# Performance work log

Hardware: AMD Instinct MI355X
Metric: run time of the kernel (lower is better)

Reference implementation:

```python
import jax, jax.numpy as jnp
import numpy as np

EMB_DIM = 1024
NUM_HEADS = 16
HEAD_DIM = EMB_DIM // NUM_HEADS


def setup_inputs() -> dict:
    key = jax.random.key(0)
    ks = jax.random.split(key, 9)
    B, S = 2, 2048
    s = 1.0 / np.sqrt(EMB_DIM)
    return {
        "x": jax.random.normal(ks[0], (B, S, EMB_DIM), jnp.float32),
        "Wq": jax.random.normal(ks[1], (EMB_DIM, EMB_DIM), jnp.float32) * s,
        "bq": jnp.zeros((EMB_DIM,), jnp.float32),
        "Wk": jax.random.normal(ks[2], (EMB_DIM, EMB_DIM), jnp.float32) * s,
        "bk": jnp.zeros((EMB_DIM,), jnp.float32),
        "Wv": jax.random.normal(ks[3], (EMB_DIM, EMB_DIM), jnp.float32) * s,
        "bv": jnp.zeros((EMB_DIM,), jnp.float32),
        "Wo": jax.random.normal(ks[4], (EMB_DIM, EMB_DIM), jnp.float32) * s,
        "bo": jnp.zeros((EMB_DIM,), jnp.float32),
    }


def reference(x, Wq, bq, Wk, bk, Wv, bv, Wo, bo):
    B, S, E = x.shape
    H, D = NUM_HEADS, HEAD_DIM
    # QKV projections (torch Linear: x @ W.T + b; here W is stored as [in,out])
    q = (x @ Wq + bq).reshape(B, S, H, D).transpose(0, 2, 1, 3)  # [B,H,S,D]
    k = (x @ Wk + bk).reshape(B, S, H, D).transpose(0, 2, 1, 3)
    v = (x @ Wv + bv).reshape(B, S, H, D).transpose(0, 2, 1, 3)
    # raw scores, then causal mask with -inf, then scale inside softmax
    scores = jnp.einsum("bhqd,bhkd->bhqk", q, k)  # [B,H,S,S]
    causal = jnp.tril(jnp.ones((S, S), bool))
    scores = jnp.where(causal, scores, -jnp.inf)
    attn = jax.nn.softmax(scores / np.sqrt(D), axis=-1)
    # dropout prob is 0.0 (eval-equivalent), so it's identity
    ctx = jnp.einsum("bhqk,bhkd->bhqd", attn, v)  # [B,H,S,D]
    ctx = ctx.transpose(0, 2, 1, 3).reshape(B, S, E)
    return ctx @ Wo + bo
```

## Files before the change

### kernel.cpp

```cpp
#include <hip/hip_runtime.h>
#include <hip/hip_bf16.h>
#include <cstdint>

#define NB   2
#define NS   2048
#define NE   1024
#define NH   16
#define ND   64
#define BS   (NB*NS)

typedef float f32x4 __attribute__((ext_vector_type(4)));
typedef __bf16 bf16x8 __attribute__((ext_vector_type(8)));

#define MFMA16(a,b,c) __builtin_amdgcn_mfma_f32_16x16x32_bf16((a),(b),(c),0,0,0)

#define KCF 0.18033688011112042f

typedef const __attribute__((address_space(1))) unsigned int* gas_u32;
typedef __attribute__((address_space(3))) unsigned int* las_u32;

__device__ __forceinline__ void gload_lds16(const void* g, void* l) {
    __builtin_amdgcn_global_load_lds((gas_u32)g, (las_u32)l, 16, 0, 0);
}

__device__ __forceinline__ unsigned short bf16_bits(float f) {
    __bf16 h = (__bf16)f;
    return __builtin_bit_cast(unsigned short, h);
}
__device__ __forceinline__ float bits_bf16(unsigned short u) {
    return (float)__builtin_bit_cast(__bf16, u);
}

__global__ __launch_bounds__(256) void prep_kernel(const float* __restrict__ x,
                                                   __bf16* __restrict__ xb,
                                                   const float* __restrict__ W0,
                                                   const float* __restrict__ W1,
                                                   const float* __restrict__ W2,
                                                   const float* __restrict__ W3,
                                                   __bf16* __restrict__ wt) {
    __shared__ float tile[32][33];
    int z = blockIdx.z;
    int tx = threadIdx.x, ty = threadIdx.y;
    if (z == 0) {
        size_t base = ((size_t)(blockIdx.y * 32 + blockIdx.x) * 256 +
                       ty * 32 + tx) * 16;
        const float4* p = (const float4*)(x + base);
        float4 a = p[0], b = p[1], c = p[2], d = p[3];
        bf16x8 v0, v1;
        v0[0]=(__bf16)a.x; v0[1]=(__bf16)a.y; v0[2]=(__bf16)a.z; v0[3]=(__bf16)a.w;
        v0[4]=(__bf16)b.x; v0[5]=(__bf16)b.y; v0[6]=(__bf16)b.z; v0[7]=(__bf16)b.w;
        v1[0]=(__bf16)c.x; v1[1]=(__bf16)c.y; v1[2]=(__bf16)c.z; v1[3]=(__bf16)c.w;
        v1[4]=(__bf16)d.x; v1[5]=(__bf16)d.y; v1[6]=(__bf16)d.z; v1[7]=(__bf16)d.w;
        *(bf16x8*)(xb + base) = v0;
        *(bf16x8*)(xb + base + 8) = v1;
        return;
    }
    int w = z - 1;
    const float* W = (w==0) ? W0 : (w==1) ? W1 : (w==2) ? W2 : W3;
    __bf16* out = wt + (size_t)w * NE * NE;
    int k0 = blockIdx.y * 32, n0 = blockIdx.x * 32;
    #pragma unroll
    for (int i = 0; i < 4; i++)
        tile[ty + 8*i][tx] = W[(size_t)(k0 + ty + 8*i) * NE + n0 + tx];
    __syncthreads();
    #pragma unroll
    for (int i = 0; i < 4; i++)
        out[(size_t)(n0 + ty + 8*i) * NE + k0 + tx] = (__bf16)tile[tx][ty + 8*i];
}

template<int EPI>
__global__ __launch_bounds__(256, 2) void gemm128_kernel(
        const __bf16* __restrict__ A, const __bf16* __restrict__ Bt,
        const float* __restrict__ bias0, const float* __restrict__ bias1,
        const float* __restrict__ bias2,
        __bf16* __restrict__ o0, __bf16* __restrict__ o1, __bf16* __restrict__ o2,
        float* __restrict__ fout) {
    __shared__ __align__(16) char smem[2][16384];
    const int K = 1024;
    int t = threadIdx.x;
    int wave = t >> 6, lane = t & 63;
    int wm = wave >> 1, wn = wave & 1;
    int lg = lane >> 4, li = lane & 15;

    int bid = blockIdx.y * gridDim.x + blockIdx.x;
    int cpx = (gridDim.x * gridDim.y) >> 3;
    int swzb = (bid & 7) * cpx + (bid >> 3);
    int m0 = (swzb / gridDim.x) * 128, n0 = (swzb % gridDim.x) * 128;

    const __bf16* Ag = A + (size_t)(m0 + (t >> 2)) * K + (t & 3) * 8;
    const __bf16* Bg = Bt + (size_t)(n0 + (t >> 2)) * K + (t & 3) * 8;

#define GSTAGE(K0, BI) do {                                             \
        gload_lds16(Ag + (K0),          smem[BI] +         t * 16);     \
        gload_lds16(Ag + 64 * K + (K0), smem[BI] +  4096 + t * 16);     \
        gload_lds16(Bg + (K0),          smem[BI] +  8192 + t * 16);     \
        gload_lds16(Bg + 64 * K + (K0), smem[BI] + 12288 + t * 16);     \
    } while (0)

    GSTAGE(0, 0);
    f32x4 acc[4][4] = {};
    __syncthreads();

    for (int k0 = 0; k0 < K; k0 += 32) {
        int cur = (k0 >> 5) & 1;
        if (k0 + 32 < K) {
            GSTAGE(k0 + 32, cur ^ 1);
            asm volatile("s_waitcnt vmcnt(4)" ::: "memory");
        } else {
            asm volatile("s_waitcnt vmcnt(0)" ::: "memory");
        }
        __builtin_amdgcn_s_barrier();

        const __bf16* As = (const __bf16*)smem[cur];
        const __bf16* Bs = (const __bf16*)(smem[cur] + 8192);
        bf16x8 af[4], bfr[4];
        #pragma unroll
        for (int i = 0; i < 4; i++)
            af[i] = *(const bf16x8*)(As + (size_t)(wm*64 + i*16 + li) * 32 + lg * 8);
        #pragma unroll
        for (int i = 0; i < 4; i++)
            bfr[i] = *(const bf16x8*)(Bs + (size_t)(wn*64 + i*16 + li) * 32 + lg * 8);
        #pragma unroll
        for (int i = 0; i < 4; i++)
            #pragma unroll
            for (int j = 0; j < 4; j++)
                acc[i][j] = MFMA16(af[i], bfr[j], acc[i][j]);

        asm volatile("s_waitcnt lgkmcnt(0)" ::: "memory");
        __builtin_amdgcn_sched_barrier(0);
        __builtin_amdgcn_s_barrier();
    }
#undef GSTAGE

    #pragma unroll
    for (int i = 0; i < 4; i++) {
        int mrow = m0 + wm * 64 + i * 16 + lg * 4;
        #pragma unroll
        for (int j = 0; j < 4; j++) {
            int n = n0 + wn * 64 + j * 16 + li;
            if (EPI == 0) {
                int widx = n >> 10, nn = n & 1023;
                const float* bb = (widx == 0) ? bias0 : (widx == 1) ? bias1 : bias2;
                float bv = bb[nn];
                int h = nn >> 6, d = nn & 63;
                int bidx = mrow >> 11, s0 = mrow & 2047;
                if (widx == 2) {
                    ushort4 pk;
                    pk.x = bf16_bits(acc[i][j][0] + bv);
                    pk.y = bf16_bits(acc[i][j][1] + bv);
                    pk.z = bf16_bits(acc[i][j][2] + bv);
                    pk.w = bf16_bits(acc[i][j][3] + bv);
                    *(ushort4*)(o2 + (((size_t)bidx * NH + h) * ND + d) * NS + s0) = pk;
                } else {
                    __bf16* dst = (widx == 0) ? o0 : o1;
                    float scl = (widx == 0) ? KCF : 1.0f;
                    #pragma unroll
                    for (int r = 0; r < 4; r++)
                        dst[(((size_t)bidx * NH + h) * NS + s0 + r) * ND + d] =
                            (__bf16)((acc[i][j][r] + bv) * scl);
                }
            } else {
                float bv = bias0[n];
                #pragma unroll
                for (int r = 0; r < 4; r++)
                    fout[(size_t)(mrow + r) * NE + n] = acc[i][j][r] + bv;
            }
        }
    }
}

__global__ __launch_bounds__(256) void attn_kernel(const __bf16* __restrict__ qb,
                                                   const __bf16* __restrict__ kb,
                                                   const __bf16* __restrict__ vt,
                                                   __bf16* __restrict__ ctx,
                                                   __bf16* __restrict__ Opart,
                                                   float* __restrict__ lbuf,
                                                   int split) {
    __shared__ __align__(16) char kbuf[2][8192];
    __shared__ __align__(16) char vbuf[2][8192];
    __shared__ __align__(16) ushort pbuf[4][1024];

    int t = threadIdx.x;
    int wave = t >> 6, lane = t & 63;
    int lg = lane >> 4, li = lane & 15;
    int bh = blockIdx.y, b = bh >> 4, h = bh & 15;
    int bx = (split ? 79 : 31) - blockIdx.x;

    int qt, c, nch;
    if (!split) {
        qt = bx; c = 0; nch = 1;
    } else {
        int a = (bx < 8) ? 0 : (bx < 24) ? 1 : (bx < 48) ? 2 : 3;
        int seg = (a == 0) ? 0 : (a == 1) ? 8 : (a == 2) ? 24 : 48;
        int idx = bx - seg;
        int dv = a + 1;
        qt = a * 8 + idx / dv;
        c  = idx % dv;
        nch = a + 1;
    }
    int jlo = c * 8;
    int jhi = min(jlo + 8, qt + 1);
    int nt = jhi - jlo;
    bool direct = (nch == 1);

    int qw = qt * 64 + wave * 16;
    const __bf16* Q  = qb + ((size_t)bh * NS + qw) * ND;
    const __bf16* Kg = kb + (size_t)bh * NS * ND;
    const __bf16* Vg = vt + (size_t)bh * ND * NS;

    int sr = t >> 3;
    int sg = (t & 7) ^ (sr & 7);
    const __bf16* Ks0 = Kg + (size_t)sr * ND + sg * 8;
    const __bf16* Ks1 = Kg + (size_t)(32 + sr) * ND + sg * 8;
    const __bf16* Vs0 = Vg + (size_t)sr * NS + sg * 8;
    const __bf16* Vs1 = Vg + (size_t)(32 + sr) * NS + sg * 8;

#define STAGE_KV(J, BI) do {                                              \
        gload_lds16(Ks0 + (size_t)(J) * 4096, &kbuf[BI][t * 16]);         \
        gload_lds16(Ks1 + (size_t)(J) * 4096, &kbuf[BI][4096 + t * 16]);  \
        gload_lds16(Vs0 + (size_t)(J) * 64,   &vbuf[BI][t * 16]);         \
        gload_lds16(Vs1 + (size_t)(J) * 64,   &vbuf[BI][4096 + t * 16]);  \
    } while (0)

    bf16x8 aq0 = *(const bf16x8*)(Q + li * ND + lg * 8);
    bf16x8 aq1 = *(const bf16x8*)(Q + li * ND + 32 + lg * 8);

    STAGE_KV(jlo, 0);

    f32x4 o[4] = {};
    float lpart = 0.f;
    int swz = (li & 7) << 4;
    int qg = qw + li;

    char* pw = (char*)&pbuf[wave][0];
    char* pwr = pw + li * 128 + (lg & 1) * 8;
    int k6base = (lg >> 1);

    __syncthreads();

    for (int it = 0; it < nt; ++it) {
        int j = jlo + it;
        int cur = it & 1;
        if (it + 1 < nt) {
            STAGE_KV(j + 1, cur ^ 1);
            asm volatile("s_waitcnt vmcnt(4)" ::: "memory");
        } else {
            asm volatile("s_waitcnt vmcnt(0)" ::: "memory");
        }
        __builtin_amdgcn_s_barrier();

        const char* kt = (const char*)kbuf[cur];
        f32x4 sc[4];
        __builtin_amdgcn_s_setprio(1);
        #pragma unroll
        for (int h4 = 0; h4 < 4; ++h4) {
            const char* kr = kt + (h4 * 16 + li) * 128;
            bf16x8 b0 = *(const bf16x8*)(kr + ((lg << 4) ^ swz));
            bf16x8 b1 = *(const bf16x8*)(kr + (((4 + lg) << 4) ^ swz));
            f32x4 z = {};
            z = MFMA16(b0, aq0, z);
            z = MFMA16(b1, aq1, z);
            sc[h4] = z;
        }
        __builtin_amdgcn_s_setprio(0);

        if (j == qt) {
            #pragma unroll
            for (int h4 = 0; h4 < 4; ++h4)
                #pragma unroll
                for (int r = 0; r < 4; ++r) {
                    int kv = j * 64 + h4 * 16 + lg * 4 + r;
                    if (kv > qg) sc[h4][r] = -1e30f;
                }
        }

        #pragma unroll
        for (int h4 = 0; h4 < 4; ++h4) {
            #pragma unroll
            for (int r = 0; r < 4; ++r) {
                float p = exp2f(sc[h4][r]);
                sc[h4][r] = p;
                lpart += p;
            }
        }

        #pragma unroll
        for (int h4 = 0; h4 < 4; ++h4) {
            uint2 w64;
            w64.x = (unsigned int)bf16_bits(sc[h4][0]) |
                    ((unsigned int)bf16_bits(sc[h4][1]) << 16);
            w64.y = (unsigned int)bf16_bits(sc[h4][2]) |
                    ((unsigned int)bf16_bits(sc[h4][3]) << 16);
            int k6 = h4 * 2 + k6base;
            *(uint2*)(pwr + (((k6 ^ (li & 7)) << 4))) = w64;
        }
        asm volatile("s_waitcnt lgkmcnt(0)" ::: "memory");
        __builtin_amdgcn_sched_barrier(0);

        const char* vtl = (const char*)vbuf[cur];
        __builtin_amdgcn_s_setprio(1);
        #pragma unroll
        for (int ks = 0; ks < 2; ++ks) {
            int ch = (ks * 4 + lg) << 4;
            bf16x8 pf = *(const bf16x8*)(pw + li * 128 + (ch ^ swz));
            #pragma unroll
            for (int i = 0; i < 4; ++i) {
                bf16x8 vf = *(const bf16x8*)(vtl + (i * 16 + li) * 128 + (ch ^ swz));
                o[i] = MFMA16(vf, pf, o[i]);
            }
        }
        __builtin_amdgcn_s_setprio(0);

        asm volatile("s_waitcnt lgkmcnt(0)" ::: "memory");
        __builtin_amdgcn_sched_barrier(0);
        __builtin_amdgcn_s_barrier();
    }
#undef STAGE_KV

    float lsum = lpart + __shfl_xor(lpart, 16);
    lsum += __shfl_xor(lsum, 32);

    if (direct) {
        float inv = 1.f / lsum;
        __bf16* dst = ctx + ((size_t)b * NS + qg) * NE + h * ND;
        #pragma unroll
        for (int i = 0; i < 4; ++i) {
            ushort4 pack;
            pack.x = bf16_bits(o[i][0] * inv);
            pack.y = bf16_bits(o[i][1] * inv);
            pack.z = bf16_bits(o[i][2] * inv);
            pack.w = bf16_bits(o[i][3] * inv);
            *(ushort4*)(dst + i * 16 + lg * 4) = pack;
        }
    } else {
        int slot = bh * 80 + bx;
        int ql = wave * 16 + li;
        __bf16* Op = Opart + (size_t)slot * 4096 + ql * 64;
        #pragma unroll
        for (int i = 0; i < 4; ++i) {
            ushort4 pack;
            pack.x = bf16_bits(o[i][0]);
            pack.y = bf16_bits(o[i][1]);
            pack.z = bf16_bits(o[i][2]);
            pack.w = bf16_bits(o[i][3]);
            *(ushort4*)(Op + i * 16 + lg * 4) = pack;
        }
        if (lg == 0)
            lbuf[(size_t)slot * 64 + ql] = lsum;
    }
}

__global__ __launch_bounds__(256) void combine_kernel(const __bf16* __restrict__ Opart,
                                                      const float* __restrict__ lbuf,
                                                      __bf16* __restrict__ ctx) {
    int qt = 8 + blockIdx.x;
    int bh = blockIdx.y, b = bh >> 4, h = bh & 15;
    int a = qt >> 3, bq = qt & 7;
    int off = (a + 1) * (4 * a + bq);
    int nch = a + 1;
    int slotbase = bh * 80 + off;
    int t = threadIdx.x;
    int q = t >> 2, dg = t & 3;

    float L = 0.f;
    #pragma unroll
    for (int c = 0; c < 4; ++c)
        if (c < nch)
            L += lbuf[(size_t)(slotbase + c) * 64 + q];
    float invL = 1.f / L;

    float acc[16] = {};
    #pragma unroll
    for (int c = 0; c < 4; ++c)
        if (c < nch) {
            const uint4* src = (const uint4*)(Opart + (size_t)(slotbase + c) * 4096 +
                                              q * 64 + dg * 16);
            #pragma unroll
            for (int half = 0; half < 2; ++half) {
                uint4 v = src[half];
                unsigned int w[4] = {v.x, v.y, v.z, v.w};
                #pragma unroll
                for (int u = 0; u < 4; ++u) {
                    acc[half * 8 + u * 2]     += bits_bf16((ushort)(w[u] & 0xffff));
                    acc[half * 8 + u * 2 + 1] += bits_bf16((ushort)(w[u] >> 16));
                }
            }
        }

    int qg = qt * 64 + q;
    __bf16* dst = ctx + ((size_t)b * NS + qg) * NE + h * ND + dg * 16;
    #pragma unroll
    for (int half = 0; half < 2; ++half) {
        ushort4 pack;
        pack.x = bf16_bits(acc[half * 8 + 0] * invL);
        pack.y = bf16_bits(acc[half * 8 + 1] * invL);
        pack.z = bf16_bits(acc[half * 8 + 2] * invL);
        pack.w = bf16_bits(acc[half * 8 + 3] * invL);
        ushort4 pack2;
        pack2.x = bf16_bits(acc[half * 8 + 4] * invL);
        pack2.y = bf16_bits(acc[half * 8 + 5] * invL);
        pack2.z = bf16_bits(acc[half * 8 + 6] * invL);
        pack2.w = bf16_bits(acc[half * 8 + 7] * invL);
        *(ushort4*)(dst + half * 8) = pack;
        *(ushort4*)(dst + half * 8 + 4) = pack2;
    }
}

extern "C" void kernel_launch(void* const* d_in, const int* in_sizes, int n_in,
                              void* d_out, int out_size, void* d_ws, size_t ws_size,
                              hipStream_t stream) {
    (void)in_sizes; (void)n_in; (void)out_size;
    const float* x  = (const float*)d_in[0];
    const float* Wq = (const float*)d_in[1];
    const float* bq = (const float*)d_in[2];
    const float* Wk = (const float*)d_in[3];
    const float* bk = (const float*)d_in[4];
    const float* Wv = (const float*)d_in[5];
    const float* bv = (const float*)d_in[6];
    const float* Wo = (const float*)d_in[7];
    const float* bo = (const float*)d_in[8];
    float* out = (float*)d_out;

    char* ws = (char*)d_ws;
    const size_t MB = 1024 * 1024;
    __bf16* xb  = (__bf16*)(ws);
    __bf16* wt  = (__bf16*)(ws +  8 * MB);
    __bf16* qb  = (__bf16*)(ws + 16 * MB);
    __bf16* kb  = (__bf16*)(ws + 24 * MB);
    __bf16* vtb = (__bf16*)(ws + 32 * MB);
    __bf16* ctx = xb;
    __bf16* Opart = (__bf16*)(ws + 40 * MB);
    float*  lbuf  = (float*)(ws + 40 * MB + 20971520);
    const size_t NEED = 40 * MB + 20971520 + 655360;

    int split = (ws_size >= NEED) ? 1 : 0;

    prep_kernel<<<dim3(32, 32, 5), dim3(32, 8), 0, stream>>>(
        x, xb, Wq, Wk, Wv, Wo, wt);
    gemm128_kernel<0><<<dim3(24, 32), 256, 0, stream>>>(
        xb, wt, bq, bk, bv, qb, kb, vtb, nullptr);
    attn_kernel<<<dim3(split ? 80 : 32, NB * NH), 256, 0, stream>>>(
        qb, kb, vtb, ctx, Opart, lbuf, split);
    if (split)
        combine_kernel<<<dim3(24, NB * NH), 256, 0, stream>>>(Opart, lbuf, ctx);
    gemm128_kernel<1><<<dim3(8, 32), 256, 0, stream>>>(
        ctx, wt + 3 * (size_t)NE * NE, bo, nullptr, nullptr, nullptr, nullptr,
        nullptr, out);
}
```

Measured before the change: 194.8 us.

## Double attention query tile per wave and split out-projection into 64-row GEMM

The attention kernel now processes 128 query rows per block (32 per wave, two MFMA row groups), so each staged K/V tile is reused across twice as many queries. The split-KV scheme, partial buffers and combine kernel are resized to match, and the causal mask test now checks each tile against the wave's rows. The output projection gets its own 64x128-tile GEMM kernel, which launches twice as many blocks to fill more CUs. The trade-off is higher register and LDS use in attention, fewer attention blocks, and more masked work on the diagonal tiles.

```diff
diff --git a/kernel.cpp b/kernel.cpp
--- a/kernel.cpp
+++ b/kernel.cpp
@@ -68,13 +68,11 @@
         out[(size_t)(n0 + ty + 8*i) * NE + k0 + tx] = (__bf16)tile[tx][ty + 8*i];
 }
 
-template<int EPI>
-__global__ __launch_bounds__(256, 2) void gemm128_kernel(
+__global__ __launch_bounds__(256, 2) void gemm_qkv_kernel(
         const __bf16* __restrict__ A, const __bf16* __restrict__ Bt,
         const float* __restrict__ bias0, const float* __restrict__ bias1,
         const float* __restrict__ bias2,
-        __bf16* __restrict__ o0, __bf16* __restrict__ o1, __bf16* __restrict__ o2,
-        float* __restrict__ fout) {
+        __bf16* __restrict__ o0, __bf16* __restrict__ o1, __bf16* __restrict__ o2) {
     __shared__ __align__(16) char smem[2][16384];
     const int K = 1024;
     int t = threadIdx.x;
@@ -138,33 +136,98 @@
         #pragma unroll
         for (int j = 0; j < 4; j++) {
             int n = n0 + wn * 64 + j * 16 + li;
-            if (EPI == 0) {
-                int widx = n >> 10, nn = n & 1023;
-                const float* bb = (widx == 0) ? bias0 : (widx == 1) ? bias1 : bias2;
-                float bv = bb[nn];
-                int h = nn >> 6, d = nn & 63;
-                int bidx = mrow >> 11, s0 = mrow & 2047;
-                if (widx == 2) {
-                    ushort4 pk;
-                    pk.x = bf16_bits(acc[i][j][0] + bv);
-                    pk.y = bf16_bits(acc[i][j][1] + bv);
-                    pk.z = bf16_bits(acc[i][j][2] + bv);
-                    pk.w = bf16_bits(acc[i][j][3] + bv);
-                    *(ushort4*)(o2 + (((size_t)bidx * NH + h) * ND + d) * NS + s0) = pk;
-                } else {
-                    __bf16* dst = (widx == 0) ? o0 : o1;
-                    float scl = (widx == 0) ? KCF : 1.0f;
-                    #pragma unroll
-                    for (int r = 0; r < 4; r++)
-                        dst[(((size_t)bidx * NH + h) * NS + s0 + r) * ND + d] =
-                            (__bf16)((acc[i][j][r] + bv) * scl);
-                }
+            int widx = n >> 10, nn = n & 1023;
+            const float* bb = (widx == 0) ? bias0 : (widx == 1) ? bias1 : bias2;
+            float bv = bb[nn];
+            int h = nn >> 6, d = nn & 63;
+            int bidx = mrow >> 11, s0 = mrow & 2047;
+            if (widx == 2) {
+                ushort4 pk;
+                pk.x = bf16_bits(acc[i][j][0] + bv);
+                pk.y = bf16_bits(acc[i][j][1] + bv);
+                pk.z = bf16_bits(acc[i][j][2] + bv);
+                pk.w = bf16_bits(acc[i][j][3] + bv);
+                *(ushort4*)(o2 + (((size_t)bidx * NH + h) * ND + d) * NS + s0) = pk;
             } else {
-                float bv = bias0[n];
+                __bf16* dst = (widx == 0) ? o0 : o1;
+                float scl = (widx == 0) ? KCF : 1.0f;
                 #pragma unroll
                 for (int r = 0; r < 4; r++)
-                    fout[(size_t)(mrow + r) * NE + n] = acc[i][j][r] + bv;
-            }
+                    dst[(((size_t)bidx * NH + h) * NS + s0 + r) * ND + d] =
+                        (__bf16)((acc[i][j][r] + bv) * scl);
+            }
+        }
+    }
+}
+
+__global__ __launch_bounds__(256, 2) void gemm_out_kernel(
+        const __bf16* __restrict__ A, const __bf16* __restrict__ Bt,
+        const float* __restrict__ bias, float* __restrict__ fout) {
+    __shared__ __align__(16) char smem[2][12288];
+    const int K = 1024;
+    int t = threadIdx.x;
+    int wave = t >> 6, lane = t & 63;
+    int lg = lane >> 4, li = lane & 15;
+
+    int bid = blockIdx.y * gridDim.x + blockIdx.x;
+    int cpx = (gridDim.x * gridDim.y) >> 3;
+    int swzb = (bid & 7) * cpx + (bid >> 3);
+    int m0 = (swzb / gridDim.x) * 64, n0 = (swzb % gridDim.x) * 128;
+
+    const __bf16* Ag = A + (size_t)(m0 + (t >> 2)) * K + (t & 3) * 8;
+    const __bf16* Bg = Bt + (size_t)(n0 + (t >> 2)) * K + (t & 3) * 8;
+
+#define GSTAGE(K0, BI) do {                                             \
+        gload_lds16(Ag + (K0),          smem[BI] +         t * 16);     \
+        gload_lds16(Bg + (K0),          smem[BI] +  4096 + t * 16);     \
+        gload_lds16(Bg + 64 * K + (K0), smem[BI] +  8192 + t * 16);     \
+    } while (0)
+
+    GSTAGE(0, 0);
+    f32x4 acc[4][2] = {};
+    __syncthreads();
+
+    for (int k0 = 0; k0 < K; k0 += 32) {
+        int cur = (k0 >> 5) & 1;
+        if (k0 + 32 < K) {
+            GSTAGE(k0 + 32, cur ^ 1);
+            asm volatile("s_waitcnt vmcnt(3)" ::: "memory");
+        } else {
+            asm volatile("s_waitcnt vmcnt(0)" ::: "memory");
+        }
+        __builtin_amdgcn_s_barrier();
+
+        const __bf16* As = (const __bf16*)smem[cur];
+        const __bf16* Bs = (const __bf16*)(smem[cur] + 4096);
+        bf16x8 af[4], bfr[2];
+        #pragma unroll
+        for (int i = 0; i < 4; i++)
+            af[i] = *(const bf16x8*)(As + (size_t)(i*16 + li) * 32 + lg * 8);
+        #pragma unroll
+        for (int j = 0; j < 2; j++)
+            bfr[j] = *(const bf16x8*)(Bs + (size_t)(wave*32 + j*16 + li) * 32 + lg * 8);
+        #pragma unroll
+        for (int i = 0; i < 4; i++)
+            #pragma unroll
+            for (int j = 0; j < 2; j++)
+                acc[i][j] = MFMA16(af[i], bfr[j], acc[i][j]);
+
+        asm volatile("s_waitcnt lgkmcnt(0)" ::: "memory");
+        __builtin_amdgcn_sched_barrier(0);
+        __builtin_amdgcn_s_barrier();
+    }
+#undef GSTAGE
+
+    #pragma unroll
+    for (int i = 0; i < 4; i++) {
+        int mrow = m0 + i * 16 + lg * 4;
+        #pragma unroll
+        for (int j = 0; j < 2; j++) {
+            int n = n0 + wave * 32 + j * 16 + li;
+            float bv = bias[n];
+            #pragma unroll
+            for (int r = 0; r < 4; r++)
+                fout[(size_t)(mrow + r) * NE + n] = acc[i][j][r] + bv;
         }
     }
 }
@@ -178,32 +241,33 @@
                                                    int split) {
     __shared__ __align__(16) char kbuf[2][8192];
     __shared__ __align__(16) char vbuf[2][8192];
-    __shared__ __align__(16) ushort pbuf[4][1024];
+    __shared__ __align__(16) ushort pbuf[4][2048];
 
     int t = threadIdx.x;
     int wave = t >> 6, lane = t & 63;
     int lg = lane >> 4, li = lane & 15;
     int bh = blockIdx.y, b = bh >> 4, h = bh & 15;
-    int bx = (split ? 79 : 31) - blockIdx.x;
-
-    int qt, c, nch;
+
+    int qtile, c, nch, slot = 0;
     if (!split) {
-        qt = bx; c = 0; nch = 1;
+        qtile = 15 - blockIdx.x; c = 0; nch = 1;
     } else {
-        int a = (bx < 8) ? 0 : (bx < 24) ? 1 : (bx < 48) ? 2 : 3;
-        int seg = (a == 0) ? 0 : (a == 1) ? 8 : (a == 2) ? 24 : 48;
+        int bx = 39 - blockIdx.x;
+        int a = (bx < 4) ? 0 : (bx < 12) ? 1 : (bx < 24) ? 2 : 3;
+        int seg = (a == 0) ? 0 : (a == 1) ? 4 : (a == 2) ? 12 : 24;
         int idx = bx - seg;
         int dv = a + 1;
-        qt = a * 8 + idx / dv;
-        c  = idx % dv;
-        nch = a + 1;
+        qtile = a * 4 + idx / dv;
+        c = idx % dv;
+        nch = dv;
+        slot = bh * 40 + bx;
     }
     int jlo = c * 8;
-    int jhi = min(jlo + 8, qt + 1);
+    int jhi = min(jlo + 8, 2 * (qtile + 1));
     int nt = jhi - jlo;
     bool direct = (nch == 1);
 
-    int qw = qt * 64 + wave * 16;
+    int qw = qtile * 128 + wave * 32;
     const __bf16* Q  = qb + ((size_t)bh * NS + qw) * ND;
     const __bf16* Kg = kb + (size_t)bh * NS * ND;
     const __bf16* Vg = vt + (size_t)bh * ND * NS;
@@ -222,18 +286,23 @@
         gload_lds16(Vs1 + (size_t)(J) * 64,   &vbuf[BI][4096 + t * 16]);  \
     } while (0)
 
-    bf16x8 aq0 = *(const bf16x8*)(Q + li * ND + lg * 8);
-    bf16x8 aq1 = *(const bf16x8*)(Q + li * ND + 32 + lg * 8);
+    bf16x8 aq[2][2];
+    #pragma unroll
+    for (int qh = 0; qh < 2; ++qh) {
+        aq[qh][0] = *(const bf16x8*)(Q + (qh * 16 + li) * ND + lg * 8);
+        aq[qh][1] = *(const bf16x8*)(Q + (qh * 16 + li) * ND + 32 + lg * 8);
+    }
 
     STAGE_KV(jlo, 0);
 
-    f32x4 o[4] = {};
-    float lpart = 0.f;
+    f32x4 o[4][2] = {};
+    float lpart[2] = {0.f, 0.f};
     int swz = (li & 7) << 4;
-    int qg = qw + li;
+    int qg0 = qw + li, qg1 = qw + 16 + li;
 
     char* pw = (char*)&pbuf[wave][0];
-    char* pwr = pw + li * 128 + (lg & 1) * 8;
+    char* pwr0 = pw + li * 128 + (lg & 1) * 8;
+    char* pwr1 = pw + (16 + li) * 128 + (lg & 1) * 8;
     int k6base = (lg >> 1);
 
     __syncthreads();
@@ -250,49 +319,57 @@
         __builtin_amdgcn_s_barrier();
 
         const char* kt = (const char*)kbuf[cur];
-        f32x4 sc[4];
+        f32x4 sc[4][2];
         __builtin_amdgcn_s_setprio(1);
         #pragma unroll
         for (int h4 = 0; h4 < 4; ++h4) {
             const char* kr = kt + (h4 * 16 + li) * 128;
             bf16x8 b0 = *(const bf16x8*)(kr + ((lg << 4) ^ swz));
             bf16x8 b1 = *(const bf16x8*)(kr + (((4 + lg) << 4) ^ swz));
-            f32x4 z = {};
-            z = MFMA16(b0, aq0, z);
-            z = MFMA16(b1, aq1, z);
-            sc[h4] = z;
+            #pragma unroll
+            for (int qh = 0; qh < 2; ++qh) {
+                f32x4 z = {};
+                z = MFMA16(b0, aq[qh][0], z);
+                z = MFMA16(b1, aq[qh][1], z);
+                sc[h4][qh] = z;
+            }
         }
         __builtin_amdgcn_s_setprio(0);
 
-        if (j == qt) {
+        if ((j << 6) + 63 > qw) {
             #pragma unroll
             for (int h4 = 0; h4 < 4; ++h4)
                 #pragma unroll
                 for (int r = 0; r < 4; ++r) {
-                    int kv = j * 64 + h4 * 16 + lg * 4 + r;
-                    if (kv > qg) sc[h4][r] = -1e30f;
+                    int kv = (j << 6) + h4 * 16 + lg * 4 + r;
+                    if (kv > qg0) sc[h4][0][r] = -1e30f;
+                    if (kv > qg1) sc[h4][1][r] = -1e30f;
                 }
         }
 
         #pragma unroll
+        for (int h4 = 0; h4 < 4; ++h4)
+            #pragma unroll
+            for (int qh = 0; qh < 2; ++qh)
+                #pragma unroll
+                for (int r = 0; r < 4; ++r) {
+                    float p = exp2f(sc[h4][qh][r]);
+                    sc[h4][qh][r] = p;
+                    lpart[qh] += p;
+                }
+
+        #pragma unroll
         for (int h4 = 0; h4 < 4; ++h4) {
-            #pragma unroll
-            for (int r = 0; r < 4; ++r) {
-                float p = exp2f(sc[h4][r]);
-                sc[h4][r] = p;
-                lpart += p;
-            }
-        }
-
-        #pragma unroll
-        for (int h4 = 0; h4 < 4; ++h4) {
-            uint2 w64;
-            w64.x = (unsigned int)bf16_bits(sc[h4][0]) |
-                    ((unsigned int)bf16_bits(sc[h4][1]) << 16);
-            w64.y = (unsigned int)bf16_bits(sc[h4][2]) |
-                    ((unsigned int)bf16_bits(sc[h4][3]) << 16);
-            int k6 = h4 * 2 + k6base;
-            *(uint2*)(pwr + (((k6 ^ (li & 7)) << 4))) = w64;
+            int chs = ((h4 * 2 + k6base) ^ (li & 7)) << 4;
+            #pragma unroll
+            for (int qh = 0; qh < 2; ++qh) {
+                uint2 w64;
+                w64.x = (unsigned int)bf16_bits(sc[h4][qh][0]) |
+                        ((unsigned int)bf16_bits(sc[h4][qh][1]) << 16);
+                w64.y = (unsigned int)bf16_bits(sc[h4][qh][2]) |
+                        ((unsigned int)bf16_bits(sc[h4][qh][3]) << 16);
+                *(uint2*)((qh ? pwr1 : pwr0) + chs) = w64;
+            }
         }
         asm volatile("s_waitcnt lgkmcnt(0)" ::: "memory");
         __builtin_amdgcn_sched_barrier(0);
@@ -301,12 +378,14 @@
         __builtin_amdgcn_s_setprio(1);
         #pragma unroll
         for (int ks = 0; ks < 2; ++ks) {
-            int ch = (ks * 4 + lg) << 4;
-            bf16x8 pf = *(const bf16x8*)(pw + li * 128 + (ch ^ swz));
+            int ch = ((ks * 4 + lg) << 4) ^ swz;
+            bf16x8 pf0 = *(const bf16x8*)(pw + li * 128 + ch);
+            bf16x8 pf1 = *(const bf16x8*)(pw + (16 + li) * 128 + ch);
             #pragma unroll
             for (int i = 0; i < 4; ++i) {
-                bf16x8 vf = *(const bf16x8*)(vtl + (i * 16 + li) * 128 + (ch ^ swz));
-                o[i] = MFMA16(vf, pf, o[i]);
+                bf16x8 vf = *(const bf16x8*)(vtl + (i * 16 + li) * 128 + ch);
+                o[i][0] = MFMA16(vf, pf0, o[i][0]);
+                o[i][1] = MFMA16(vf, pf1, o[i][1]);
             }
         }
         __builtin_amdgcn_s_setprio(0);
@@ -317,92 +396,101 @@
     }
 #undef STAGE_KV
 
-    float lsum = lpart + __shfl_xor(lpart, 16);
-    lsum += __shfl_xor(lsum, 32);
+    float lsum[2];
+    #pragma unroll
+    for (int qh = 0; qh < 2; ++qh) {
+        float v = lpart[qh] + __shfl_xor(lpart[qh], 16);
+        lsum[qh] = v + __shfl_xor(v, 32);
+    }
 
     if (direct) {
-        float inv = 1.f / lsum;
-        __bf16* dst = ctx + ((size_t)b * NS + qg) * NE + h * ND;
-        #pragma unroll
-        for (int i = 0; i < 4; ++i) {
-            ushort4 pack;
-            pack.x = bf16_bits(o[i][0] * inv);
-            pack.y = bf16_bits(o[i][1] * inv);
-            pack.z = bf16_bits(o[i][2] * inv);
-            pack.w = bf16_bits(o[i][3] * inv);
-            *(ushort4*)(dst + i * 16 + lg * 4) = pack;
+        #pragma unroll
+        for (int qh = 0; qh < 2; ++qh) {
+            float inv = 1.f / lsum[qh];
+            int qg = qw + qh * 16 + li;
+            __bf16* dst = ctx + ((size_t)b * NS + qg) * NE + h * ND;
+            #pragma unroll
+            for (int i = 0; i < 4; ++i) {
+                ushort4 pack;
+                pack.x = bf16_bits(o[i][qh][0] * inv);
+                pack.y = bf16_bits(o[i][qh][1] * inv);
+                pack.z = bf16_bits(o[i][qh][2] * inv);
+                pack.w = bf16_bits(o[i][qh][3] * inv);
+                *(ushort4*)(dst + i * 16 + lg * 4) = pack;
+            }
         }
     } else {
-        int slot = bh * 80 + bx;
-        int ql = wave * 16 + li;
-        __bf16* Op = Opart + (size_t)slot * 4096 + ql * 64;
-        #pragma unroll
-        for (int i = 0; i < 4; ++i) {
-            ushort4 pack;
-            pack.x = bf16_bits(o[i][0]);
-            pack.y = bf16_bits(o[i][1]);
-            pack.z = bf16_bits(o[i][2]);
-            pack.w = bf16_bits(o[i][3]);
-            *(ushort4*)(Op + i * 16 + lg * 4) = pack;
-        }
-        if (lg == 0)
-            lbuf[(size_t)slot * 64 + ql] = lsum;
+        #pragma unroll
+        for (int qh = 0; qh < 2; ++qh) {
+            int ql = wave * 32 + qh * 16 + li;
+            __bf16* Op = Opart + (size_t)slot * 8192 + ql * 64;
+            #pragma unroll
+            for (int i = 0; i < 4; ++i) {
+                ushort4 pack;
+                pack.x = bf16_bits(o[i][qh][0]);
+                pack.y = bf16_bits(o[i][qh][1]);
+                pack.z = bf16_bits(o[i][qh][2]);
+                pack.w = bf16_bits(o[i][qh][3]);
+                *(ushort4*)(Op + i * 16 + lg * 4) = pack;
+            }
+            if (lg == 0)
+                lbuf[(size_t)slot * 128 + ql] = lsum[qh];
+        }
     }
 }
 
 __global__ __launch_bounds__(256) void combine_kernel(const __bf16* __restrict__ Opart,
                                                       const float* __restrict__ lbuf,
                                                       __bf16* __restrict__ ctx) {
-    int qt = 8 + blockIdx.x;
+    int i = 4 + blockIdx.x;
     int bh = blockIdx.y, b = bh >> 4, h = bh & 15;
-    int a = qt >> 3, bq = qt & 7;
-    int off = (a + 1) * (4 * a + bq);
+    int a = i >> 2;
+    int slotbase = bh * 40 + (a + 1) * (i - 2 * a);
     int nch = a + 1;
-    int slotbase = bh * 80 + off;
     int t = threadIdx.x;
-    int q = t >> 2, dg = t & 3;
+    int q = t >> 1, dh = (t & 1) * 32;
 
     float L = 0.f;
     #pragma unroll
     for (int c = 0; c < 4; ++c)
         if (c < nch)
-            L += lbuf[(size_t)(slotbase + c) * 64 + q];
+            L += lbuf[(size_t)(slotbase + c) * 128 + q];
     float invL = 1.f / L;
 
-    float acc[16] = {};
+    float acc[32] = {};
     #pragma unroll
     for (int c = 0; c < 4; ++c)
         if (c < nch) {
-            const uint4* src = (const uint4*)(Opart + (size_t)(slotbase + c) * 4096 +
-                                              q * 64 + dg * 16);
-            #pragma unroll
-            for (int half = 0; half < 2; ++half) {
-                uint4 v = src[half];
+            const uint4* src = (const uint4*)(Opart + (size_t)(slotbase + c) * 8192 +
+                                              q * 64 + dh);
+            #pragma unroll
+            for (int g = 0; g < 4; ++g) {
+                uint4 v = src[g];
                 unsigned int w[4] = {v.x, v.y, v.z, v.w};
                 #pragma unroll
                 for (int u = 0; u < 4; ++u) {
-                    acc[half * 8 + u * 2]     += bits_bf16((ushort)(w[u] & 0xffff));
-                    acc[half * 8 + u * 2 + 1] += bits_bf16((ushort)(w[u] >> 16));
+                    acc[g * 8 + u * 2]     += bits_bf16((ushort)(w[u] & 0xffff));
+                    acc[g * 8 + u * 2 + 1] += bits_bf16((ushort)(w[u] >> 16));
                 }
             }
         }
 
-    int qg = qt * 64 + q;
-    __bf16* dst = ctx + ((size_t)b * NS + qg) * NE + h * ND + dg * 16;
-    #pragma unroll
-    for (int half = 0; half < 2; ++half) {
-        ushort4 pack;
-        pack.x = bf16_bits(acc[half * 8 + 0] * invL);
-        pack.y = bf16_bits(acc[half * 8 + 1] * invL);
-        pack.z = bf16_bits(acc[half * 8 + 2] * invL);
-        pack.w = bf16_bits(acc[half * 8 + 3] * invL);
-        ushort4 pack2;
-        pack2.x = bf16_bits(acc[half * 8 + 4] * invL);
-        pack2.y = bf16_bits(acc[half * 8 + 5] * invL);
-        pack2.z = bf16_bits(acc[half * 8 + 6] * invL);
-        pack2.w = bf16_bits(acc[half * 8 + 7] * invL);
-        *(ushort4*)(dst + half * 8) = pack;
-        *(ushort4*)(dst + half * 8 + 4) = pack2;
+    int qg = i * 128 + q;
+    __bf16* dst = ctx + ((size_t)b * NS + qg) * NE + h * ND + dh;
+    #pragma unroll
+    for (int g = 0; g < 4; ++g) {
+        ushort4 pk;
+        pk.x = bf16_bits(acc[g * 8 + 0] * invL);
+        pk.y = bf16_bits(acc[g * 8 + 1] * invL);
+        pk.z = bf16_bits(acc[g * 8 + 2] * invL);
+        pk.w = bf16_bits(acc[g * 8 + 3] * invL);
+        ushort4 pk2;
+        pk2.x = bf16_bits(acc[g * 8 + 4] * invL);
+        pk2.y = bf16_bits(acc[g * 8 + 5] * invL);
+        pk2.z = bf16_bits(acc[g * 8 + 6] * invL);
+        pk2.w = bf16_bits(acc[g * 8 + 7] * invL);
+        *(ushort4*)(dst + g * 8) = pk;
+        *(ushort4*)(dst + g * 8 + 4) = pk2;
     }
 }
 
@@ -437,13 +525,12 @@
 
     prep_kernel<<<dim3(32, 32, 5), dim3(32, 8), 0, stream>>>(
         x, xb, Wq, Wk, Wv, Wo, wt);
-    gemm128_kernel<0><<<dim3(24, 32), 256, 0, stream>>>(
-        xb, wt, bq, bk, bv, qb, kb, vtb, nullptr);
-    attn_kernel<<<dim3(split ? 80 : 32, NB * NH), 256, 0, stream>>>(
+    gemm_qkv_kernel<<<dim3(24, 32), 256, 0, stream>>>(
+        xb, wt, bq, bk, bv, qb, kb, vtb);
+    attn_kernel<<<dim3(split ? 40 : 16, NB * NH), 256, 0, stream>>>(
         qb, kb, vtb, ctx, Opart, lbuf, split);
     if (split)
-        combine_kernel<<<dim3(24, NB * NH), 256, 0, stream>>>(Opart, lbuf, ctx);
-    gemm128_kernel<1><<<dim3(8, 32), 256, 0, stream>>>(
-        ctx, wt + 3 * (size_t)NE * NE, bo, nullptr, nullptr, nullptr, nullptr,
-        nullptr, out);
-}
+        combine_kernel<<<dim3(12, NB * NH), 256, 0, stream>>>(Opart, lbuf, ctx);
+    gemm_out_kernel<<<dim3(8, 64), 256, 0, stream>>>(
+        ctx, wt + 3 * (size_t)NE * NE, bo, out);
+}
```

Result: slower. 200.1 us (+2.7%).
